# Kernel optimization log

Hardware: AMD Instinct MI355X
Metric: run time of the kernel (lower is better)

The kernel has to match this reference:

```python
import jax, jax.numpy as jnp
import numpy as np

_DN = ('NDHWC', 'DHWIO', 'NDHWC')

def _deconv(x, w, b, stride):
    # kernel-3 transposed conv; SAME padding -> out spatial = in * stride
    y = jax.lax.conv_transpose(x, w, strides=(stride, stride, stride),
                               padding='SAME', dimension_numbers=_DN)
    return y + b


def setup_inputs() -> dict:
    key = jax.random.key(0)
    ks = jax.random.split(key, 14)
    C = 128

    def w(k, cin, cout):
        std = 1.0 / np.sqrt(27.0 * cin)  # fan-in init, kernel 3^3
        return jax.random.normal(k, (3, 3, 3, cin, cout), jnp.float32) * std

    def b(k, cout):
        return jax.random.normal(k, (cout,), jnp.float32) * 0.01

    return {
        'x':   jax.random.normal(ks[0], (1, 8, 8, 8, C), jnp.float32),
        'w0':  w(ks[1], C, C),  'b0':  b(ks[2], C),
        'w00': w(ks[3], C, C),  'b00': b(ks[4], C),
        'w1':  w(ks[5], C, C),  'b1':  b(ks[6], C),
        'w10': w(ks[7], C, C),  'b10': b(ks[8], C),
        'w2':  w(ks[9], C, 64), 'b2':  b(ks[10], 64),
        'w20': w(ks[11], 64, 3), 'b20': b(ks[12], 3),
    }


def reference(x, w0, b0, w00, b00, w1, b1, w10, b10, w2, b2, w20, b20):
    # deconv0 (stride 2) -> deconv0_0 (stride 1) -> ReLU
    out = jax.nn.relu(_deconv(_deconv(x, w0, b0, 2), w00, b00, 1))
    # deconv1 (stride 2) -> deconv1_0 (stride 1) -> ReLU
    out = jax.nn.relu(_deconv(_deconv(out, w1, b1, 2), w10, b10, 1))
    # deconv2 (stride 2, C->64) -> deconv2_0 (stride 1, 64->3)
    out = _deconv(_deconv(out, w2, b2, 2), w20, b20, 1)
    return out
```

## Files before the change

### kernel.cpp

```cpp
#include <hip/hip_runtime.h>


typedef __attribute__((ext_vector_type(8))) short bf16x8;
typedef __attribute__((ext_vector_type(8))) _Float16 f16x8;
typedef __attribute__((ext_vector_type(4))) float f32x4;
typedef unsigned short u16;

__device__ __forceinline__ u16 f2bf(float f) {
    unsigned u = __builtin_bit_cast(unsigned, f);
    u += 0x7fffu + ((u >> 16) & 1u);
    return (u16)(u >> 16);
}
__device__ __forceinline__ float bf2f(u16 h) {
    unsigned u = ((unsigned)h) << 16;
    return __builtin_bit_cast(float, u);
}
__device__ __forceinline__ void split_store(float v, u16* ph, u16* pl) {
    u16 h = f2bf(v);
    *ph = h;
    *pl = f2bf(v - bf2f(h));
}
__device__ __forceinline__ u16 f2h(float v) {
    return __builtin_bit_cast(u16, (_Float16)v);
}
__device__ __forceinline__ int rfl(int v) { return __builtin_amdgcn_readfirstlane(v); }
__device__ __forceinline__ int swz(int bx, int G) { return (bx & 7) * (G >> 3) + (bx >> 3); }

__global__ __launch_bounds__(256) void pack_all(
    const float* __restrict__ x, float* __restrict__ zf,
    u16* __restrict__ Xh, u16* __restrict__ Xl,
    const float* __restrict__ w0_, const float* __restrict__ w1_,
    const float* __restrict__ w2_, const float* __restrict__ w3_,
    const float* __restrict__ w4_, const float* __restrict__ w5_,
    u16* s0h, u16* s0l, u16* s1h, u16* s1l, u16* s2h, u16* s2l,
    u16* s3h, u16* s3l, u16* s4h, u16* s4l, u16* s5h, u16* s5l)
{
    if (blockIdx.y == 6) {
        if (blockIdx.x < 64) {
            const int i = (blockIdx.x * 256 + threadIdx.x) * 4;
            const float4 v = *(const float4*)(x + i);
            split_store(v.x, Xh + i,     Xl + i);
            split_store(v.y, Xh + i + 1, Xl + i + 1);
            split_store(v.z, Xh + i + 2, Xl + i + 2);
            split_store(v.w, Xh + i + 3, Xl + i + 3);
        } else if (blockIdx.x == 64) {
            ((float4*)zf)[threadIdx.x] = make_float4(0.f, 0.f, 0.f, 0.f);
        }
        return;
    }
    const float* w; u16 *bh, *bl; int Cin, Cout, nNt;
    switch (blockIdx.y) {
        case 0: w = w0_; bh = s0h; bl = s0l; Cin = 128; Cout = 128; nNt = 8; break;
        case 1: w = w1_; bh = s1h; bl = s1l; Cin = 128; Cout = 128; nNt = 8; break;
        case 2: w = w2_; bh = s2h; bl = s2l; Cin = 128; Cout = 128; nNt = 8; break;
        case 3: w = w3_; bh = s3h; bl = s3l; Cin = 128; Cout = 128; nNt = 8; break;
        case 4: w = w4_; bh = s4h; bl = s4l; Cin = 128; Cout = 64;  nNt = 4; break;
        default:w = w5_; bh = s5h; bl = s5l; Cin = 64;  Cout = 3;   nNt = 1; break;
    }
    const bool f16 = (blockIdx.y == 5);
    const int KC = Cin >> 5;
    const int total = 27 * nNt * KC * 64;
    int t = blockIdx.x * 256 + threadIdx.x;
    if (t >= total) return;
    const int lane = t & 63;
    int r = t >> 6;
    const int kc = r % KC; r /= KC;
    const int nt = r % nNt; r /= nNt;
    const int tap = r;
    const int n  = nt * 16 + (lane & 15);
    const int k0 = kc * 32 + (lane >> 4) * 8;
    const size_t o = (size_t)t * 8;
    for (int j = 0; j < 8; ++j) {
        float v = (n < Cout) ? w[((size_t)tap * Cin + k0 + j) * Cout + n] : 0.f;
        if (f16) {
            const _Float16 h = (_Float16)v;
            bh[o + j] = __builtin_bit_cast(u16, h);
            bl[o + j] = f2h(v - (float)h);
        } else {
            const u16 h = f2bf(v);
            bh[o + j] = h;
            bl[o + j] = f2bf(v - bf2f(h));
        }
    }
}

template<int CIN, int MT, int NT, bool RELU>
__global__ __launch_bounds__(64) void conv_s1_mfma(
    const u16* __restrict__ Ah, const u16* __restrict__ Al,
    const u16* __restrict__ Bh, const u16* __restrict__ Bl,
    const float* __restrict__ bias, const u16* __restrict__ Z,
    u16* __restrict__ Yh, u16* __restrict__ Yl,
    int D, int lD, int Cout, int nNtTot)
{
    constexpr int KC = CIN >> 5;
    const int lane = threadIdx.x;
    const int ml = lane & 15, kq = lane >> 4;
    const int M0 = swz(blockIdx.x, gridDim.x) * (MT * 16);
    const int N0t = blockIdx.y * NT;

    int vw[MT], vh[MT], vd[MT];
    #pragma unroll
    for (int mt = 0; mt < MT; ++mt) {
        const int vox = M0 + mt * 16 + ml;
        vw[mt] = vox & (D - 1); vh[mt] = (vox >> lD) & (D - 1); vd[mt] = vox >> (2 * lD);
    }

    f32x4 acc[MT][NT];
    #pragma unroll
    for (int nt = 0; nt < NT; ++nt) {
        const float bv = bias[(N0t + nt) * 16 + ml];
        #pragma unroll
        for (int mt = 0; mt < MT; ++mt) acc[mt][nt] = (f32x4){bv, bv, bv, bv};
    }

    const u16 *pah[MT], *pal[MT];
    size_t fb;
    auto set_tap = [&](int tap) {
        const int kd = tap / 9, kh = (tap % 9) / 3, kw = tap % 3;
        #pragma unroll
        for (int mt = 0; mt < MT; ++mt) {
            const int id = vd[mt] + kd - 1, ih = vh[mt] + kh - 1, iw = vw[mt] + kw - 1;
            const bool v = (unsigned)id < (unsigned)D && (unsigned)ih < (unsigned)D &&
                           (unsigned)iw < (unsigned)D;
            const size_t off = (size_t)((id * D + ih) * D + iw) * CIN;
            pah[mt] = v ? Ah + off : Z;
            pal[mt] = v ? Al + off : Z;
        }
        fb = ((size_t)tap * nNtTot + N0t) * KC;
    };

    bf16x8 fah[2][MT], fal[2][MT], fbh[2][NT], fbl[2][NT];
    auto load_frags = [&](int buf, int kc) {
        const int ko = kc * 32 + kq * 8;
        #pragma unroll
        for (int mt = 0; mt < MT; ++mt) {
            fah[buf][mt] = *(const bf16x8*)(pah[mt] + ko);
            fal[buf][mt] = *(const bf16x8*)(pal[mt] + ko);
        }
        #pragma unroll
        for (int nt = 0; nt < NT; ++nt) {
            const size_t fo = (fb + (size_t)nt * KC + kc) * 512 + lane * 8;
            fbh[buf][nt] = *(const bf16x8*)(Bh + fo);
            fbl[buf][nt] = *(const bf16x8*)(Bl + fo);
        }
    };

    set_tap(0);
    load_frags(0, 0);

    for (int tap = 0; tap < 27; ++tap) {
        #pragma unroll
        for (int kc = 0; kc < KC; ++kc) {
            const int cur = kc & 1, nxt = cur ^ 1;
            if (kc + 1 < KC) {
                load_frags(nxt, kc + 1);
            } else {
                set_tap(tap < 26 ? tap + 1 : 26);
                load_frags(nxt, 0);
            }
            #pragma unroll
            for (int mt = 0; mt < MT; ++mt)
            #pragma unroll
            for (int nt = 0; nt < NT; ++nt) {
                acc[mt][nt] = __builtin_amdgcn_mfma_f32_16x16x32_bf16(fah[cur][mt], fbh[cur][nt], acc[mt][nt], 0, 0, 0);
                acc[mt][nt] = __builtin_amdgcn_mfma_f32_16x16x32_bf16(fah[cur][mt], fbl[cur][nt], acc[mt][nt], 0, 0, 0);
                acc[mt][nt] = __builtin_amdgcn_mfma_f32_16x16x32_bf16(fal[cur][mt], fbh[cur][nt], acc[mt][nt], 0, 0, 0);
            }
        }
    }

    #pragma unroll
    for (int mt = 0; mt < MT; ++mt) {
        const int vox0 = M0 + mt * 16 + kq * 4;
        #pragma unroll
        for (int nt = 0; nt < NT; ++nt) {
            const int co = (N0t + nt) * 16 + ml;
            #pragma unroll
            for (int r = 0; r < 4; ++r) {
                float v = acc[mt][nt][r];
                if (RELU) v = fmaxf(v, 0.f);
                const size_t yo = (size_t)(vox0 + r) * Cout + co;
                split_store(v, Yh + yo, Yl + yo);
            }
        }
    }
}

template<int D, int R, bool RELU>
__global__ __launch_bounds__(256) void conv_s1_lds(
    const u16* __restrict__ Ah, const u16* __restrict__ Al,
    const u16* __restrict__ Bh, const u16* __restrict__ Bl,
    const float* __restrict__ bias,
    u16* __restrict__ Yh, u16* __restrict__ Yl)
{
    constexpr int KC  = 4;
    constexpr int SH  = R + 2;
    constexpr int SW  = D + 2;
    constexpr int VST = 72;
    __shared__ u16 sm[3 * SH * SW * VST];

    const int tid  = threadIdx.x;
    const int lane = tid & 63, widx = tid >> 6;
    const int ml = lane & 15, kq = lane >> 4;

    const int bpp = D / R;
    const int lb  = swz(blockIdx.x, gridDim.x);
    const int d   = lb / bpp;
    const int h0  = (lb % bpp) * R;
    const int N0  = widx * 2;

    f32x4 acc[4][2];
    #pragma unroll
    for (int nt = 0; nt < 2; ++nt) {
        const float bv = bias[(N0 + nt) * 16 + ml];
        #pragma unroll
        for (int mt = 0; mt < 4; ++mt) acc[mt][nt] = (f32x4){bv, bv, bv, bv};
    }

    for (int i = tid; i < 3 * SH * 2 * 9; i += 256) {
        const int slot = i / 9, c8 = i % 9;
        const int side = slot & 1, rr = slot >> 1;
        const int dd = rr / SH, hh = rr % SH;
        *(bf16x8*)(sm + ((dd * SH + hh) * SW + (side ? SW - 1 : 0)) * VST + c8 * 8) =
            (bf16x8){0,0,0,0,0,0,0,0};
    }

    bf16x8 cbh[2], cbl[2], nbh[2], nbl[2];
    auto loadB = [&](bf16x8 (&dh)[2], bf16x8 (&dl)[2], int kc, int tap) {
        #pragma unroll
        for (int nt = 0; nt < 2; ++nt) {
            const size_t fo = (((size_t)tap * 8 + N0 + nt) * KC + kc) * 512 + lane * 8;
            dh[nt] = *(const bf16x8*)(Bh + fo);
            dl[nt] = *(const bf16x8*)(Bl + fo);
        }
    };
    loadB(cbh, cbl, 0, 0);

    for (int kc = 0; kc < KC; ++kc) {
        __syncthreads();
        constexpr int NCH = 3 * SH * D * 8;
        for (int i = tid; i < NCH; i += 256) {
            const int vox = i >> 3, c8 = i & 7;
            const int ww = vox % D;
            const int rr = vox / D;
            const int hh = rr % SH, dd = rr / SH;
            const int pd = d + dd - 1, ph = h0 + hh - 1;
            u16* dst = sm + ((dd * SH + hh) * SW + ww + 1) * VST + c8 * 8;
            if ((unsigned)pd < (unsigned)D && (unsigned)ph < (unsigned)D) {
                const u16* srcb = (c8 < 4) ? Ah : Al;
                const size_t g = ((size_t)(pd * D + ph) * D + ww) * 128 + kc * 32 + (c8 & 3) * 8;
                *(bf16x8*)dst = *(const bf16x8*)(srcb + g);
            } else {
                *(bf16x8*)dst = (bf16x8){0,0,0,0,0,0,0,0};
            }
        }
        __syncthreads();

        for (int tap = 0; tap < 27; ++tap) {
            const int lin = kc * 27 + tap + 1;
            if (lin < KC * 27) loadB(nbh, nbl, lin / 27, lin % 27);
            const int kd = tap / 9, kh = (tap % 9) / 3, kw = tap % 3;
            bf16x8 fa_h[4], fa_l[4];
            #pragma unroll
            for (int mt = 0; mt < 4; ++mt) {
                const int m = mt * 16 + ml;
                const int mh = m / D, mw = m % D;
                const u16* p = sm + (((kd * SH) + (mh + kh)) * SW + (mw + kw)) * VST;
                fa_h[mt] = *(const bf16x8*)(p + kq * 8);
                fa_l[mt] = *(const bf16x8*)(p + 32 + kq * 8);
            }
            #pragma unroll
            for (int mt = 0; mt < 4; ++mt)
            #pragma unroll
            for (int nt = 0; nt < 2; ++nt) {
                acc[mt][nt] = __builtin_amdgcn_mfma_f32_16x16x32_bf16(fa_h[mt], cbh[nt], acc[mt][nt], 0, 0, 0);
                acc[mt][nt] = __builtin_amdgcn_mfma_f32_16x16x32_bf16(fa_h[mt], cbl[nt], acc[mt][nt], 0, 0, 0);
                acc[mt][nt] = __builtin_amdgcn_mfma_f32_16x16x32_bf16(fa_l[mt], cbh[nt], acc[mt][nt], 0, 0, 0);
            }
            #pragma unroll
            for (int nt = 0; nt < 2; ++nt) { cbh[nt] = nbh[nt]; cbl[nt] = nbl[nt]; }
        }
    }

    const size_t M0 = (size_t)(d * D + h0) * D;
    #pragma unroll
    for (int mt = 0; mt < 4; ++mt) {
        #pragma unroll
        for (int nt = 0; nt < 2; ++nt) {
            const int co = (N0 + nt) * 16 + ml;
            #pragma unroll
            for (int r = 0; r < 4; ++r) {
                float v = acc[mt][nt][r];
                if (RELU) v = fmaxf(v, 0.f);
                const size_t yo = (M0 + mt * 16 + kq * 4 + r) * 128 + co;
                split_store(v, Yh + yo, Yl + yo);
            }
        }
    }
}

template<int CIN, int MT, int NT, bool F16OUT = false>
__global__ __launch_bounds__(64) void deconv_s2_mfma(
    const u16* __restrict__ Ah, const u16* __restrict__ Al,
    const u16* __restrict__ Bh, const u16* __restrict__ Bl,
    const float* __restrict__ bias, const u16* __restrict__ Z,
    u16* __restrict__ Yh, u16* __restrict__ Yl,
    int Din, int lD, int Cout, int nNtTot)
{
    constexpr int KC = CIN >> 5;
    const int Dout = 2 * Din;
    const int lane = threadIdx.x;
    const int ml = lane & 15, kq = lane >> 4;
    const int M0 = swz(blockIdx.x, gridDim.x) * (MT * 16);
    const int N0t = blockIdx.y * NT;
    const int par = blockIdx.z;
    const int rd = (par >> 2) & 1, rh = (par >> 1) & 1, rw = par & 1;

    int sw[MT], sh[MT], sd[MT];
    #pragma unroll
    for (int mt = 0; mt < MT; ++mt) {
        const int sv = M0 + mt * 16 + ml;
        sw[mt] = sv & (Din - 1); sh[mt] = (sv >> lD) & (Din - 1); sd[mt] = sv >> (2 * lD);
    }

    f32x4 acc[MT][NT];
    #pragma unroll
    for (int nt = 0; nt < NT; ++nt) {
        const float bv = bias[(N0t + nt) * 16 + ml];
        #pragma unroll
        for (int mt = 0; mt < MT; ++mt) acc[mt][nt] = (f32x4){bv, bv, bv, bv};
    }

    const int lw = rw ? 0 : 1, lh = rh ? 0 : 1, ld2 = rd ? 0 : 1;
    const int ntap = 1 << (lw + lh + ld2);

    const u16 *pah[MT], *pal[MT];
    size_t fb;
    auto set_tap = [&](int t) {
        const int tw_ = t & ((1 << lw) - 1);
        const int th_ = (t >> lw) & ((1 << lh) - 1);
        const int td_ = t >> (lw + lh);
        const int kd = rd ? 1 : (td_ ? 0 : 2);
        const int kh = rh ? 1 : (th_ ? 0 : 2);
        const int kw = rw ? 1 : (tw_ ? 0 : 2);
        const int dd = rd ? 0 : -td_, dh = rh ? 0 : -th_, dw = rw ? 0 : -tw_;
        const int tap = (kd * 3 + kh) * 3 + kw;
        #pragma unroll
        for (int mt = 0; mt < MT; ++mt) {
            const int id = sd[mt] + dd, ih = sh[mt] + dh, iw = sw[mt] + dw;
            const bool v = id >= 0 && ih >= 0 && iw >= 0;
            const size_t off = (size_t)((id * Din + ih) * Din + iw) * CIN;
            pah[mt] = v ? Ah + off : Z;
            pal[mt] = v ? Al + off : Z;
        }
        fb = ((size_t)tap * nNtTot + N0t) * KC;
    };

    bf16x8 fah[2][MT], fal[2][MT], fbh[2][NT], fbl[2][NT];
    auto load_frags = [&](int buf, int kc) {
        const int ko = kc * 32 + kq * 8;
        #pragma unroll
        for (int mt = 0; mt < MT; ++mt) {
            fah[buf][mt] = *(const bf16x8*)(pah[mt] + ko);
            fal[buf][mt] = *(const bf16x8*)(pal[mt] + ko);
        }
        #pragma unroll
        for (int nt = 0; nt < NT; ++nt) {
            const size_t fo = (fb + (size_t)nt * KC + kc) * 512 + lane * 8;
            fbh[buf][nt] = *(const bf16x8*)(Bh + fo);
            fbl[buf][nt] = *(const bf16x8*)(Bl + fo);
        }
    };

    set_tap(0);
    load_frags(0, 0);

    for (int t = 0; t < ntap; ++t) {
        #pragma unroll
        for (int kc = 0; kc < KC; ++kc) {
            const int cur = kc & 1, nxt = cur ^ 1;
            if (kc + 1 < KC) {
                load_frags(nxt, kc + 1);
            } else {
                set_tap(t + 1 < ntap ? t + 1 : t);
                load_frags(nxt, 0);
            }
            #pragma unroll
            for (int mt = 0; mt < MT; ++mt)
            #pragma unroll
            for (int nt = 0; nt < NT; ++nt) {
                acc[mt][nt] = __builtin_amdgcn_mfma_f32_16x16x32_bf16(fah[cur][mt], fbh[cur][nt], acc[mt][nt], 0, 0, 0);
                acc[mt][nt] = __builtin_amdgcn_mfma_f32_16x16x32_bf16(fah[cur][mt], fbl[cur][nt], acc[mt][nt], 0, 0, 0);
                acc[mt][nt] = __builtin_amdgcn_mfma_f32_16x16x32_bf16(fal[cur][mt], fbh[cur][nt], acc[mt][nt], 0, 0, 0);
            }
        }
    }

    #pragma unroll
    for (int mt = 0; mt < MT; ++mt) {
        #pragma unroll
        for (int r = 0; r < 4; ++r) {
            const int sv = M0 + mt * 16 + kq * 4 + r;
            const int svw = sv & (Din - 1), svh = (sv >> lD) & (Din - 1), svd = sv >> (2 * lD);
            const int od = 2 * svd + rd, oh = 2 * svh + rh, ow = 2 * svw + rw;
            const size_t yb = (size_t)((od * Dout + oh) * Dout + ow) * Cout;
            #pragma unroll
            for (int nt = 0; nt < NT; ++nt) {
                const int co = (N0t + nt) * 16 + ml;
                if (F16OUT) Yh[yb + co] = f2h(acc[mt][nt][r]);
                else        split_store(acc[mt][nt][r], Yh + yb + co, Yl + yb + co);
            }
        }
    }
}

#define L5_VST 40
#define L5_RST (66 * L5_VST)
__global__ __launch_bounds__(256) void conv_c3_lds(
    const u16* __restrict__ A,
    const u16* __restrict__ Bh, const u16* __restrict__ Bl,
    const float* __restrict__ bias, float* __restrict__ out)
{
    __shared__ u16 sm[6 * L5_RST];

    const int tid  = threadIdx.x;
    const int lane = tid & 63, widx = tid >> 6;
    const int ml = lane & 15, kq = lane >> 4;

    const int lb = swz(blockIdx.x, gridDim.x);
    const int d  = lb >> 4;
    const int h0 = (lb & 15) * 4;

    const float bv = (ml < 3) ? bias[ml] : 0.f;
    f32x4 acc[4];
    #pragma unroll
    for (int mt = 0; mt < 4; ++mt) acc[mt] = (f32x4){bv, bv, bv, bv};

    f16x8 cbh, cbl, nbh, nbl;
    auto loadB = [&](f16x8& dh, f16x8& dl, int tap, int kc) {
        const size_t fo = ((size_t)tap * 2 + kc) * 512 + lane * 8;
        dh = *(const f16x8*)(Bh + fo);
        dl = *(const f16x8*)(Bl + fo);
    };
    loadB(cbh, cbl, 0, 0);

    for (int kd = 0; kd < 3; ++kd) {
        const int pd = d + kd - 1;
        const bool vpd = (unsigned)pd < 64u;
        for (int kc = 0; kc < 2; ++kc) {
            __syncthreads();
            #pragma unroll
            for (int i = 0; i < 6; ++i) {
                const int c = tid + 256 * i;
                const int r = c >> 8;
                const int rem = c & 255;
                const int vox = rem >> 2, c8 = rem & 3;
                const int hh = h0 - 1 + r;
                u16* dst = sm + r * L5_RST + (vox + 1) * L5_VST + c8 * 8;
                if (vpd && (unsigned)hh < 64u) {
                    const size_t g = (size_t)((pd * 64 + hh) * 64 + vox) * 64
                                   + kc * 32 + c8 * 8;
                    *(f16x8*)dst = *(const f16x8*)(A + g);
                } else {
                    *(f16x8*)dst = (f16x8){0,0,0,0,0,0,0,0};
                }
            }
            if (tid < 48) {
                const int r = tid >> 3, side = (tid >> 2) & 1, c8 = tid & 3;
                *(f16x8*)(sm + r * L5_RST + (side ? 65 : 0) * L5_VST + c8 * 8) =
                    (f16x8){0,0,0,0,0,0,0,0};
            }
            __syncthreads();

            #pragma unroll
            for (int t = 0; t < 9; ++t) {
                {
                    int lin = (kd * 2 + kc) * 9 + t + 1;
                    if (lin > 53) lin = 53;
                    const int Pn = lin / 9, tn = lin - Pn * 9;
                    loadB(nbh, nbl, (Pn >> 1) * 9 + tn, Pn & 1);
                }
                const int kh = t / 3, kw = t - kh * 3;
                const int slot = widx + kh;
                #pragma unroll
                for (int mt = 0; mt < 4; ++mt) {
                    const u16* p = sm + slot * L5_RST + (mt * 16 + ml + kw) * L5_VST;
                    const f16x8 af = *(const f16x8*)(p + kq * 8);
                    acc[mt] = __builtin_amdgcn_mfma_f32_16x16x32_f16(af, cbh, acc[mt], 0, 0, 0);
                    acc[mt] = __builtin_amdgcn_mfma_f32_16x16x32_f16(af, cbl, acc[mt], 0, 0, 0);
                }
                cbh = nbh; cbl = nbl;
            }
        }
    }

    if (ml < 3) {
        const int h = h0 + widx;
        const size_t vb = (size_t)(d * 64 + h) * 64;
        #pragma unroll
        for (int mt = 0; mt < 4; ++mt)
        #pragma unroll
        for (int r = 0; r < 4; ++r)
            out[(vb + mt * 16 + kq * 4 + r) * 3 + ml] = acc[mt][r];
    }
}

extern "C" void kernel_launch(void* const* d_in, const int* in_sizes, int n_in,
                              void* d_out, int out_size, void* d_ws, size_t ws_size,
                              hipStream_t stream)
{
    const float* x   = (const float*)d_in[0];
    const float* w0  = (const float*)d_in[1];  const float* b0  = (const float*)d_in[2];
    const float* w00 = (const float*)d_in[3];  const float* b00 = (const float*)d_in[4];
    const float* w1  = (const float*)d_in[5];  const float* b1  = (const float*)d_in[6];
    const float* w10 = (const float*)d_in[7];  const float* b10 = (const float*)d_in[8];
    const float* w2  = (const float*)d_in[9];  const float* b2  = (const float*)d_in[10];
    const float* w20 = (const float*)d_in[11]; const float* b20 = (const float*)d_in[12];
    float* out = (float*)d_out;

    char* ws = (char*)d_ws;
    float* zf = (float*)ws;
    u16*   Z  = (u16*)ws;
    u16* S4h = (u16*)(ws + 4096);
    u16* S4l = S4h + 221184;
    u16* S5h = S4l + 221184;
    u16* S5l = S5h + 27648;
    u16* Qh  = (u16*)(ws + 1048576);
    u16* Ql  = Qh + 4194304;
    u16* Ph  = (u16*)(ws + 17825792);
    u16* Pl  = Ph + 16777216;
    u16* S1h = (u16*)(ws + 60817408);
    u16* S1l = S1h + 442368;
    u16* S2h = S1l + 442368;
    u16* S2l = S2h + 442368;
    u16* S3h = S2l + 442368;
    u16* S3l = S3h + 442368;
    u16* S0h = S3l + 442368;
    u16* S0l = S0h + 442368;
    u16* Xh  = S0l + 442368;
    u16* Xl  = Xh + 65536;

    pack_all<<<dim3(216, 7), 256, 0, stream>>>(x, zf, Xh, Xl,
        w0, w00, w1, w10, w2, w20,
        S0h, S0l, S1h, S1l, S2h, S2l, S3h, S3l, S4h, S4l, S5h, S5l);

    deconv_s2_mfma<128, 2, 4><<<dim3(16, 2, 8), 64, 0, stream>>>(
        Xh, Xl, S0h, S0l, b0, Z, Ph, Pl, 8, 3, 128, 8);

    conv_s1_mfma<128, 1, 2, true><<<dim3(256, 4), 64, 0, stream>>>(
        Ph, Pl, S1h, S1l, b00, Z, Qh, Ql, 16, 4, 128, 8);

    deconv_s2_mfma<128, 2, 4><<<dim3(128, 2, 8), 64, 0, stream>>>(
        Qh, Ql, S2h, S2l, b1, Z, Ph, Pl, 16, 4, 128, 8);

    conv_s1_lds<32, 2, true><<<dim3(512), 256, 0, stream>>>(
        Ph, Pl, S3h, S3l, b10, Qh, Ql);

    deconv_s2_mfma<128, 4, 4, true><<<dim3(512, 1, 8), 64, 0, stream>>>(
        Qh, Ql, S4h, S4l, b2, Z, Ph, Pl, 32, 5, 64, 4);

    conv_c3_lds<<<dim3(1024), 256, 0, stream>>>(Ph, S5h, S5l, b20, out);
}
```

Before: 369.9 us.

## Switch intermediate activations to single fp16 with split fp16 weights

Intermediate activations between layers are now stored as one fp16 array instead of a bf16 hi/lo pair. Weights for layers 1-5 are packed as fp16 hi/lo. Each K step now issues two f16 MFMAs instead of three bf16 MFMAs, and activation loads, stores and LDS staging are halved. The cost is lower activation precision (fp16 mantissa and range instead of about 16-bit split bf16), which could affect accuracy.

```diff
diff --git a/kernel.cpp b/kernel.cpp
--- a/kernel.cpp
+++ b/kernel.cpp
@@ -23,7 +23,6 @@
 __device__ __forceinline__ u16 f2h(float v) {
     return __builtin_bit_cast(u16, (_Float16)v);
 }
-__device__ __forceinline__ int rfl(int v) { return __builtin_amdgcn_readfirstlane(v); }
 __device__ __forceinline__ int swz(int bx, int G) { return (bx & 7) * (G >> 3) + (bx >> 3); }
 
 __global__ __launch_bounds__(256) void pack_all(
@@ -57,7 +56,7 @@
         case 4: w = w4_; bh = s4h; bl = s4l; Cin = 128; Cout = 64;  nNt = 4; break;
         default:w = w5_; bh = s5h; bl = s5l; Cin = 64;  Cout = 3;   nNt = 1; break;
     }
-    const bool f16 = (blockIdx.y == 5);
+    const bool f16 = (blockIdx.y >= 1);
     const int KC = Cin >> 5;
     const int total = 27 * nNt * KC * 64;
     int t = blockIdx.x * 256 + threadIdx.x;
@@ -84,228 +83,12 @@
     }
 }
 
-template<int CIN, int MT, int NT, bool RELU>
-__global__ __launch_bounds__(64) void conv_s1_mfma(
+template<int CIN, int MT, int NT>
+__global__ __launch_bounds__(64) void deconv_s2_bf16(
     const u16* __restrict__ Ah, const u16* __restrict__ Al,
     const u16* __restrict__ Bh, const u16* __restrict__ Bl,
     const float* __restrict__ bias, const u16* __restrict__ Z,
-    u16* __restrict__ Yh, u16* __restrict__ Yl,
-    int D, int lD, int Cout, int nNtTot)
-{
-    constexpr int KC = CIN >> 5;
-    const int lane = threadIdx.x;
-    const int ml = lane & 15, kq = lane >> 4;
-    const int M0 = swz(blockIdx.x, gridDim.x) * (MT * 16);
-    const int N0t = blockIdx.y * NT;
-
-    int vw[MT], vh[MT], vd[MT];
-    #pragma unroll
-    for (int mt = 0; mt < MT; ++mt) {
-        const int vox = M0 + mt * 16 + ml;
-        vw[mt] = vox & (D - 1); vh[mt] = (vox >> lD) & (D - 1); vd[mt] = vox >> (2 * lD);
-    }
-
-    f32x4 acc[MT][NT];
-    #pragma unroll
-    for (int nt = 0; nt < NT; ++nt) {
-        const float bv = bias[(N0t + nt) * 16 + ml];
-        #pragma unroll
-        for (int mt = 0; mt < MT; ++mt) acc[mt][nt] = (f32x4){bv, bv, bv, bv};
-    }
-
-    const u16 *pah[MT], *pal[MT];
-    size_t fb;
-    auto set_tap = [&](int tap) {
-        const int kd = tap / 9, kh = (tap % 9) / 3, kw = tap % 3;
-        #pragma unroll
-        for (int mt = 0; mt < MT; ++mt) {
-            const int id = vd[mt] + kd - 1, ih = vh[mt] + kh - 1, iw = vw[mt] + kw - 1;
-            const bool v = (unsigned)id < (unsigned)D && (unsigned)ih < (unsigned)D &&
-                           (unsigned)iw < (unsigned)D;
-            const size_t off = (size_t)((id * D + ih) * D + iw) * CIN;
-            pah[mt] = v ? Ah + off : Z;
-            pal[mt] = v ? Al + off : Z;
-        }
-        fb = ((size_t)tap * nNtTot + N0t) * KC;
-    };
-
-    bf16x8 fah[2][MT], fal[2][MT], fbh[2][NT], fbl[2][NT];
-    auto load_frags = [&](int buf, int kc) {
-        const int ko = kc * 32 + kq * 8;
-        #pragma unroll
-        for (int mt = 0; mt < MT; ++mt) {
-            fah[buf][mt] = *(const bf16x8*)(pah[mt] + ko);
-            fal[buf][mt] = *(const bf16x8*)(pal[mt] + ko);
-        }
-        #pragma unroll
-        for (int nt = 0; nt < NT; ++nt) {
-            const size_t fo = (fb + (size_t)nt * KC + kc) * 512 + lane * 8;
-            fbh[buf][nt] = *(const bf16x8*)(Bh + fo);
-            fbl[buf][nt] = *(const bf16x8*)(Bl + fo);
-        }
-    };
-
-    set_tap(0);
-    load_frags(0, 0);
-
-    for (int tap = 0; tap < 27; ++tap) {
-        #pragma unroll
-        for (int kc = 0; kc < KC; ++kc) {
-            const int cur = kc & 1, nxt = cur ^ 1;
-            if (kc + 1 < KC) {
-                load_frags(nxt, kc + 1);
-            } else {
-                set_tap(tap < 26 ? tap + 1 : 26);
-                load_frags(nxt, 0);
-            }
-            #pragma unroll
-            for (int mt = 0; mt < MT; ++mt)
-            #pragma unroll
-            for (int nt = 0; nt < NT; ++nt) {
-                acc[mt][nt] = __builtin_amdgcn_mfma_f32_16x16x32_bf16(fah[cur][mt], fbh[cur][nt], acc[mt][nt], 0, 0, 0);
-                acc[mt][nt] = __builtin_amdgcn_mfma_f32_16x16x32_bf16(fah[cur][mt], fbl[cur][nt], acc[mt][nt], 0, 0, 0);
-                acc[mt][nt] = __builtin_amdgcn_mfma_f32_16x16x32_bf16(fal[cur][mt], fbh[cur][nt], acc[mt][nt], 0, 0, 0);
-            }
-        }
-    }
-
-    #pragma unroll
-    for (int mt = 0; mt < MT; ++mt) {
-        const int vox0 = M0 + mt * 16 + kq * 4;
-        #pragma unroll
-        for (int nt = 0; nt < NT; ++nt) {
-            const int co = (N0t + nt) * 16 + ml;
-            #pragma unroll
-            for (int r = 0; r < 4; ++r) {
-                float v = acc[mt][nt][r];
-                if (RELU) v = fmaxf(v, 0.f);
-                const size_t yo = (size_t)(vox0 + r) * Cout + co;
-                split_store(v, Yh + yo, Yl + yo);
-            }
-        }
-    }
-}
-
-template<int D, int R, bool RELU>
-__global__ __launch_bounds__(256) void conv_s1_lds(
-    const u16* __restrict__ Ah, const u16* __restrict__ Al,
-    const u16* __restrict__ Bh, const u16* __restrict__ Bl,
-    const float* __restrict__ bias,
-    u16* __restrict__ Yh, u16* __restrict__ Yl)
-{
-    constexpr int KC  = 4;
-    constexpr int SH  = R + 2;
-    constexpr int SW  = D + 2;
-    constexpr int VST = 72;
-    __shared__ u16 sm[3 * SH * SW * VST];
-
-    const int tid  = threadIdx.x;
-    const int lane = tid & 63, widx = tid >> 6;
-    const int ml = lane & 15, kq = lane >> 4;
-
-    const int bpp = D / R;
-    const int lb  = swz(blockIdx.x, gridDim.x);
-    const int d   = lb / bpp;
-    const int h0  = (lb % bpp) * R;
-    const int N0  = widx * 2;
-
-    f32x4 acc[4][2];
-    #pragma unroll
-    for (int nt = 0; nt < 2; ++nt) {
-        const float bv = bias[(N0 + nt) * 16 + ml];
-        #pragma unroll
-        for (int mt = 0; mt < 4; ++mt) acc[mt][nt] = (f32x4){bv, bv, bv, bv};
-    }
-
-    for (int i = tid; i < 3 * SH * 2 * 9; i += 256) {
-        const int slot = i / 9, c8 = i % 9;
-        const int side = slot & 1, rr = slot >> 1;
-        const int dd = rr / SH, hh = rr % SH;
-        *(bf16x8*)(sm + ((dd * SH + hh) * SW + (side ? SW - 1 : 0)) * VST + c8 * 8) =
-            (bf16x8){0,0,0,0,0,0,0,0};
-    }
-
-    bf16x8 cbh[2], cbl[2], nbh[2], nbl[2];
-    auto loadB = [&](bf16x8 (&dh)[2], bf16x8 (&dl)[2], int kc, int tap) {
-        #pragma unroll
-        for (int nt = 0; nt < 2; ++nt) {
-            const size_t fo = (((size_t)tap * 8 + N0 + nt) * KC + kc) * 512 + lane * 8;
-            dh[nt] = *(const bf16x8*)(Bh + fo);
-            dl[nt] = *(const bf16x8*)(Bl + fo);
-        }
-    };
-    loadB(cbh, cbl, 0, 0);
-
-    for (int kc = 0; kc < KC; ++kc) {
-        __syncthreads();
-        constexpr int NCH = 3 * SH * D * 8;
-        for (int i = tid; i < NCH; i += 256) {
-            const int vox = i >> 3, c8 = i & 7;
-            const int ww = vox % D;
-            const int rr = vox / D;
-            const int hh = rr % SH, dd = rr / SH;
-            const int pd = d + dd - 1, ph = h0 + hh - 1;
-            u16* dst = sm + ((dd * SH + hh) * SW + ww + 1) * VST + c8 * 8;
-            if ((unsigned)pd < (unsigned)D && (unsigned)ph < (unsigned)D) {
-                const u16* srcb = (c8 < 4) ? Ah : Al;
-                const size_t g = ((size_t)(pd * D + ph) * D + ww) * 128 + kc * 32 + (c8 & 3) * 8;
-                *(bf16x8*)dst = *(const bf16x8*)(srcb + g);
-            } else {
-                *(bf16x8*)dst = (bf16x8){0,0,0,0,0,0,0,0};
-            }
-        }
-        __syncthreads();
-
-        for (int tap = 0; tap < 27; ++tap) {
-            const int lin = kc * 27 + tap + 1;
-            if (lin < KC * 27) loadB(nbh, nbl, lin / 27, lin % 27);
-            const int kd = tap / 9, kh = (tap % 9) / 3, kw = tap % 3;
-            bf16x8 fa_h[4], fa_l[4];
-            #pragma unroll
-            for (int mt = 0; mt < 4; ++mt) {
-                const int m = mt * 16 + ml;
-                const int mh = m / D, mw = m % D;
-                const u16* p = sm + (((kd * SH) + (mh + kh)) * SW + (mw + kw)) * VST;
-                fa_h[mt] = *(const bf16x8*)(p + kq * 8);
-                fa_l[mt] = *(const bf16x8*)(p + 32 + kq * 8);
-            }
-            #pragma unroll
-            for (int mt = 0; mt < 4; ++mt)
-            #pragma unroll
-            for (int nt = 0; nt < 2; ++nt) {
-                acc[mt][nt] = __builtin_amdgcn_mfma_f32_16x16x32_bf16(fa_h[mt], cbh[nt], acc[mt][nt], 0, 0, 0);
-                acc[mt][nt] = __builtin_amdgcn_mfma_f32_16x16x32_bf16(fa_h[mt], cbl[nt], acc[mt][nt], 0, 0, 0);
-                acc[mt][nt] = __builtin_amdgcn_mfma_f32_16x16x32_bf16(fa_l[mt], cbh[nt], acc[mt][nt], 0, 0, 0);
-            }
-            #pragma unroll
-            for (int nt = 0; nt < 2; ++nt) { cbh[nt] = nbh[nt]; cbl[nt] = nbl[nt]; }
-        }
-    }
-
-    const size_t M0 = (size_t)(d * D + h0) * D;
-    #pragma unroll
-    for (int mt = 0; mt < 4; ++mt) {
-        #pragma unroll
-        for (int nt = 0; nt < 2; ++nt) {
-            const int co = (N0 + nt) * 16 + ml;
-            #pragma unroll
-            for (int r = 0; r < 4; ++r) {
-                float v = acc[mt][nt][r];
-                if (RELU) v = fmaxf(v, 0.f);
-                const size_t yo = (M0 + mt * 16 + kq * 4 + r) * 128 + co;
-                split_store(v, Yh + yo, Yl + yo);
-            }
-        }
-    }
-}
-
-template<int CIN, int MT, int NT, bool F16OUT = false>
-__global__ __launch_bounds__(64) void deconv_s2_mfma(
-    const u16* __restrict__ Ah, const u16* __restrict__ Al,
-    const u16* __restrict__ Bh, const u16* __restrict__ Bl,
-    const float* __restrict__ bias, const u16* __restrict__ Z,
-    u16* __restrict__ Yh, u16* __restrict__ Yl,
-    int Din, int lD, int Cout, int nNtTot)
+    u16* __restrict__ Y, int Din, int lD, int Cout, int nNtTot)
 {
     constexpr int KC = CIN >> 5;
     const int Dout = 2 * Din;
@@ -405,10 +188,313 @@
             const int od = 2 * svd + rd, oh = 2 * svh + rh, ow = 2 * svw + rw;
             const size_t yb = (size_t)((od * Dout + oh) * Dout + ow) * Cout;
             #pragma unroll
+            for (int nt = 0; nt < NT; ++nt)
+                Y[yb + (N0t + nt) * 16 + ml] = f2h(acc[mt][nt][r]);
+        }
+    }
+}
+
+template<int CIN, int MT, int NT, bool RELU>
+__global__ __launch_bounds__(64) void conv_s1_f16(
+    const u16* __restrict__ A, const u16* __restrict__ Bh, const u16* __restrict__ Bl,
+    const float* __restrict__ bias, const u16* __restrict__ Z,
+    u16* __restrict__ Y, int D, int lD, int Cout, int nNtTot)
+{
+    constexpr int KC = CIN >> 5;
+    const int lane = threadIdx.x;
+    const int ml = lane & 15, kq = lane >> 4;
+    const int M0 = swz(blockIdx.x, gridDim.x) * (MT * 16);
+    const int N0t = blockIdx.y * NT;
+
+    int vw[MT], vh[MT], vd[MT];
+    #pragma unroll
+    for (int mt = 0; mt < MT; ++mt) {
+        const int vox = M0 + mt * 16 + ml;
+        vw[mt] = vox & (D - 1); vh[mt] = (vox >> lD) & (D - 1); vd[mt] = vox >> (2 * lD);
+    }
+
+    f32x4 acc[MT][NT];
+    #pragma unroll
+    for (int nt = 0; nt < NT; ++nt) {
+        const float bv = bias[(N0t + nt) * 16 + ml];
+        #pragma unroll
+        for (int mt = 0; mt < MT; ++mt) acc[mt][nt] = (f32x4){bv, bv, bv, bv};
+    }
+
+    const u16* pa[MT];
+    size_t fb;
+    auto set_tap = [&](int tap) {
+        const int kd = tap / 9, kh = (tap % 9) / 3, kw = tap % 3;
+        #pragma unroll
+        for (int mt = 0; mt < MT; ++mt) {
+            const int id = vd[mt] + kd - 1, ih = vh[mt] + kh - 1, iw = vw[mt] + kw - 1;
+            const bool v = (unsigned)id < (unsigned)D && (unsigned)ih < (unsigned)D &&
+                           (unsigned)iw < (unsigned)D;
+            pa[mt] = v ? A + (size_t)((id * D + ih) * D + iw) * CIN : Z;
+        }
+        fb = ((size_t)tap * nNtTot + N0t) * KC;
+    };
+
+    f16x8 fa[2][MT], fbh[2][NT], fbl[2][NT];
+    auto load_frags = [&](int buf, int kc) {
+        const int ko = kc * 32 + kq * 8;
+        #pragma unroll
+        for (int mt = 0; mt < MT; ++mt)
+            fa[buf][mt] = *(const f16x8*)(pa[mt] + ko);
+        #pragma unroll
+        for (int nt = 0; nt < NT; ++nt) {
+            const size_t fo = (fb + (size_t)nt * KC + kc) * 512 + lane * 8;
+            fbh[buf][nt] = *(const f16x8*)(Bh + fo);
+            fbl[buf][nt] = *(const f16x8*)(Bl + fo);
+        }
+    };
+
+    set_tap(0);
+    load_frags(0, 0);
+
+    for (int tap = 0; tap < 27; ++tap) {
+        #pragma unroll
+        for (int kc = 0; kc < KC; ++kc) {
+            const int cur = kc & 1, nxt = cur ^ 1;
+            if (kc + 1 < KC) {
+                load_frags(nxt, kc + 1);
+            } else {
+                set_tap(tap < 26 ? tap + 1 : 26);
+                load_frags(nxt, 0);
+            }
+            #pragma unroll
+            for (int mt = 0; mt < MT; ++mt)
+            #pragma unroll
             for (int nt = 0; nt < NT; ++nt) {
-                const int co = (N0t + nt) * 16 + ml;
-                if (F16OUT) Yh[yb + co] = f2h(acc[mt][nt][r]);
-                else        split_store(acc[mt][nt][r], Yh + yb + co, Yl + yb + co);
+                acc[mt][nt] = __builtin_amdgcn_mfma_f32_16x16x32_f16(fa[cur][mt], fbh[cur][nt], acc[mt][nt], 0, 0, 0);
+                acc[mt][nt] = __builtin_amdgcn_mfma_f32_16x16x32_f16(fa[cur][mt], fbl[cur][nt], acc[mt][nt], 0, 0, 0);
+            }
+        }
+    }
+
+    #pragma unroll
+    for (int mt = 0; mt < MT; ++mt) {
+        const int vox0 = M0 + mt * 16 + kq * 4;
+        #pragma unroll
+        for (int nt = 0; nt < NT; ++nt) {
+            const int co = (N0t + nt) * 16 + ml;
+            #pragma unroll
+            for (int r = 0; r < 4; ++r) {
+                float v = acc[mt][nt][r];
+                if (RELU) v = fmaxf(v, 0.f);
+                Y[(size_t)(vox0 + r) * Cout + co] = f2h(v);
+            }
+        }
+    }
+}
+
+template<int CIN, int MT, int NT>
+__global__ __launch_bounds__(64) void deconv_s2_f16(
+    const u16* __restrict__ A, const u16* __restrict__ Bh, const u16* __restrict__ Bl,
+    const float* __restrict__ bias, const u16* __restrict__ Z,
+    u16* __restrict__ Y, int Din, int lD, int Cout, int nNtTot)
+{
+    constexpr int KC = CIN >> 5;
+    const int Dout = 2 * Din;
+    const int lane = threadIdx.x;
+    const int ml = lane & 15, kq = lane >> 4;
+    const int M0 = swz(blockIdx.x, gridDim.x) * (MT * 16);
+    const int N0t = blockIdx.y * NT;
+    const int par = blockIdx.z;
+    const int rd = (par >> 2) & 1, rh = (par >> 1) & 1, rw = par & 1;
+
+    int sw[MT], sh[MT], sd[MT];
+    #pragma unroll
+    for (int mt = 0; mt < MT; ++mt) {
+        const int sv = M0 + mt * 16 + ml;
+        sw[mt] = sv & (Din - 1); sh[mt] = (sv >> lD) & (Din - 1); sd[mt] = sv >> (2 * lD);
+    }
+
+    f32x4 acc[MT][NT];
+    #pragma unroll
+    for (int nt = 0; nt < NT; ++nt) {
+        const float bv = bias[(N0t + nt) * 16 + ml];
+        #pragma unroll
+        for (int mt = 0; mt < MT; ++mt) acc[mt][nt] = (f32x4){bv, bv, bv, bv};
+    }
+
+    const int lw = rw ? 0 : 1, lh = rh ? 0 : 1, ld2 = rd ? 0 : 1;
+    const int ntap = 1 << (lw + lh + ld2);
+
+    const u16* pa[MT];
+    size_t fb;
+    auto set_tap = [&](int t) {
+        const int tw_ = t & ((1 << lw) - 1);
+        const int th_ = (t >> lw) & ((1 << lh) - 1);
+        const int td_ = t >> (lw + lh);
+        const int kd = rd ? 1 : (td_ ? 0 : 2);
+        const int kh = rh ? 1 : (th_ ? 0 : 2);
+        const int kw = rw ? 1 : (tw_ ? 0 : 2);
+        const int dd = rd ? 0 : -td_, dh = rh ? 0 : -th_, dw = rw ? 0 : -tw_;
+        const int tap = (kd * 3 + kh) * 3 + kw;
+        #pragma unroll
+        for (int mt = 0; mt < MT; ++mt) {
+            const int id = sd[mt] + dd, ih = sh[mt] + dh, iw = sw[mt] + dw;
+            const bool v = id >= 0 && ih >= 0 && iw >= 0;
+            pa[mt] = v ? A + (size_t)((id * Din + ih) * Din + iw) * CIN : Z;
+        }
+        fb = ((size_t)tap * nNtTot + N0t) * KC;
+    };
+
+    f16x8 fa[2][MT], fbh[2][NT], fbl[2][NT];
+    auto load_frags = [&](int buf, int kc) {
+        const int ko = kc * 32 + kq * 8;
+        #pragma unroll
+        for (int mt = 0; mt < MT; ++mt)
+            fa[buf][mt] = *(const f16x8*)(pa[mt] + ko);
+        #pragma unroll
+        for (int nt = 0; nt < NT; ++nt) {
+            const size_t fo = (fb + (size_t)nt * KC + kc) * 512 + lane * 8;
+            fbh[buf][nt] = *(const f16x8*)(Bh + fo);
+            fbl[buf][nt] = *(const f16x8*)(Bl + fo);
+        }
+    };
+
+    set_tap(0);
+    load_frags(0, 0);
+
+    for (int t = 0; t < ntap; ++t) {
+        #pragma unroll
+        for (int kc = 0; kc < KC; ++kc) {
+            const int cur = kc & 1, nxt = cur ^ 1;
+            if (kc + 1 < KC) {
+                load_frags(nxt, kc + 1);
+            } else {
+                set_tap(t + 1 < ntap ? t + 1 : t);
+                load_frags(nxt, 0);
+            }
+            #pragma unroll
+            for (int mt = 0; mt < MT; ++mt)
+            #pragma unroll
+            for (int nt = 0; nt < NT; ++nt) {
+                acc[mt][nt] = __builtin_amdgcn_mfma_f32_16x16x32_f16(fa[cur][mt], fbh[cur][nt], acc[mt][nt], 0, 0, 0);
+                acc[mt][nt] = __builtin_amdgcn_mfma_f32_16x16x32_f16(fa[cur][mt], fbl[cur][nt], acc[mt][nt], 0, 0, 0);
+            }
+        }
+    }
+
+    #pragma unroll
+    for (int mt = 0; mt < MT; ++mt) {
+        #pragma unroll
+        for (int r = 0; r < 4; ++r) {
+            const int sv = M0 + mt * 16 + kq * 4 + r;
+            const int svw = sv & (Din - 1), svh = (sv >> lD) & (Din - 1), svd = sv >> (2 * lD);
+            const int od = 2 * svd + rd, oh = 2 * svh + rh, ow = 2 * svw + rw;
+            const size_t yb = (size_t)((od * Dout + oh) * Dout + ow) * Cout;
+            #pragma unroll
+            for (int nt = 0; nt < NT; ++nt)
+                Y[yb + (N0t + nt) * 16 + ml] = f2h(acc[mt][nt][r]);
+        }
+    }
+}
+
+template<int D, int R, bool RELU>
+__global__ __launch_bounds__(256) void conv_s1_lds_f16(
+    const u16* __restrict__ A, const u16* __restrict__ Bh, const u16* __restrict__ Bl,
+    const float* __restrict__ bias, u16* __restrict__ Y)
+{
+    constexpr int KC  = 4;
+    constexpr int SH  = R + 2;
+    constexpr int SW  = D + 2;
+    constexpr int VST = 40;
+    __shared__ u16 sm[3 * SH * SW * VST];
+
+    const int tid  = threadIdx.x;
+    const int lane = tid & 63, widx = tid >> 6;
+    const int ml = lane & 15, kq = lane >> 4;
+
+    const int bpp = D / R;
+    const int lb  = swz(blockIdx.x, gridDim.x);
+    const int d   = lb / bpp;
+    const int h0  = (lb % bpp) * R;
+    const int N0  = widx * 2;
+
+    f32x4 acc[4][2];
+    #pragma unroll
+    for (int nt = 0; nt < 2; ++nt) {
+        const float bv = bias[(N0 + nt) * 16 + ml];
+        #pragma unroll
+        for (int mt = 0; mt < 4; ++mt) acc[mt][nt] = (f32x4){bv, bv, bv, bv};
+    }
+
+    for (int i = tid; i < 3 * SH * 2 * 4; i += 256) {
+        const int slot = i >> 2, c8 = i & 3;
+        const int side = slot & 1, rr = slot >> 1;
+        const int dd = rr / SH, hh = rr % SH;
+        *(f16x8*)(sm + ((dd * SH + hh) * SW + (side ? SW - 1 : 0)) * VST + c8 * 8) =
+            (f16x8){0,0,0,0,0,0,0,0};
+    }
+
+    f16x8 cbh[2], cbl[2], nbh[2], nbl[2];
+    auto loadB = [&](f16x8 (&dh)[2], f16x8 (&dl)[2], int kc, int tap) {
+        #pragma unroll
+        for (int nt = 0; nt < 2; ++nt) {
+            const size_t fo = (((size_t)tap * 8 + N0 + nt) * KC + kc) * 512 + lane * 8;
+            dh[nt] = *(const f16x8*)(Bh + fo);
+            dl[nt] = *(const f16x8*)(Bl + fo);
+        }
+    };
+    loadB(cbh, cbl, 0, 0);
+
+    for (int kc = 0; kc < KC; ++kc) {
+        __syncthreads();
+        constexpr int NCH = 3 * SH * D * 4;
+        for (int i = tid; i < NCH; i += 256) {
+            const int vox = i >> 2, c8 = i & 3;
+            const int ww = vox % D;
+            const int rr = vox / D;
+            const int hh = rr % SH, dd = rr / SH;
+            const int pd = d + dd - 1, ph = h0 + hh - 1;
+            u16* dst = sm + ((dd * SH + hh) * SW + ww + 1) * VST + c8 * 8;
+            if ((unsigned)pd < (unsigned)D && (unsigned)ph < (unsigned)D) {
+                const size_t g = ((size_t)(pd * D + ph) * D + ww) * 128 + kc * 32 + c8 * 8;
+                *(f16x8*)dst = *(const f16x8*)(A + g);
+            } else {
+                *(f16x8*)dst = (f16x8){0,0,0,0,0,0,0,0};
+            }
+        }
+        __syncthreads();
+
+        for (int tap = 0; tap < 27; ++tap) {
+            const int lin = kc * 27 + tap + 1;
+            if (lin < KC * 27) loadB(nbh, nbl, lin / 27, lin % 27);
+            const int kd = tap / 9, kh = (tap % 9) / 3, kw = tap % 3;
+            f16x8 fa[4];
+            #pragma unroll
+            for (int mt = 0; mt < 4; ++mt) {
+                const int m = mt * 16 + ml;
+                const int mh = m / D, mw = m % D;
+                fa[mt] = *(const f16x8*)(sm + (((kd * SH) + (mh + kh)) * SW + (mw + kw)) * VST
+                                          + kq * 8);
+            }
+            #pragma unroll
+            for (int mt = 0; mt < 4; ++mt)
+            #pragma unroll
+            for (int nt = 0; nt < 2; ++nt) {
+                acc[mt][nt] = __builtin_amdgcn_mfma_f32_16x16x32_f16(fa[mt], cbh[nt], acc[mt][nt], 0, 0, 0);
+                acc[mt][nt] = __builtin_amdgcn_mfma_f32_16x16x32_f16(fa[mt], cbl[nt], acc[mt][nt], 0, 0, 0);
+            }
+            #pragma unroll
+            for (int nt = 0; nt < 2; ++nt) { cbh[nt] = nbh[nt]; cbl[nt] = nbl[nt]; }
+        }
+    }
+
+    const size_t M0 = (size_t)(d * D + h0) * D;
+    #pragma unroll
+    for (int mt = 0; mt < 4; ++mt) {
+        #pragma unroll
+        for (int nt = 0; nt < 2; ++nt) {
+            const int co = (N0 + nt) * 16 + ml;
+            #pragma unroll
+            for (int r = 0; r < 4; ++r) {
+                float v = acc[mt][nt][r];
+                if (RELU) v = fmaxf(v, 0.f);
+                Y[(M0 + mt * 16 + kq * 4 + r) * 128 + co] = f2h(v);
             }
         }
     }
@@ -544,20 +630,20 @@
         w0, w00, w1, w10, w2, w20,
         S0h, S0l, S1h, S1l, S2h, S2l, S3h, S3l, S4h, S4l, S5h, S5l);
 
-    deconv_s2_mfma<128, 2, 4><<<dim3(16, 2, 8), 64, 0, stream>>>(
-        Xh, Xl, S0h, S0l, b0, Z, Ph, Pl, 8, 3, 128, 8);
-
-    conv_s1_mfma<128, 1, 2, true><<<dim3(256, 4), 64, 0, stream>>>(
-        Ph, Pl, S1h, S1l, b00, Z, Qh, Ql, 16, 4, 128, 8);
-
-    deconv_s2_mfma<128, 2, 4><<<dim3(128, 2, 8), 64, 0, stream>>>(
-        Qh, Ql, S2h, S2l, b1, Z, Ph, Pl, 16, 4, 128, 8);
-
-    conv_s1_lds<32, 2, true><<<dim3(512), 256, 0, stream>>>(
-        Ph, Pl, S3h, S3l, b10, Qh, Ql);
-
-    deconv_s2_mfma<128, 4, 4, true><<<dim3(512, 1, 8), 64, 0, stream>>>(
-        Qh, Ql, S4h, S4l, b2, Z, Ph, Pl, 32, 5, 64, 4);
+    deconv_s2_bf16<128, 2, 4><<<dim3(16, 2, 8), 64, 0, stream>>>(
+        Xh, Xl, S0h, S0l, b0, Z, Ph, 8, 3, 128, 8);
+
+    conv_s1_f16<128, 1, 2, true><<<dim3(256, 4), 64, 0, stream>>>(
+        Ph, S1h, S1l, b00, Z, Qh, 16, 4, 128, 8);
+
+    deconv_s2_f16<128, 2, 4><<<dim3(128, 2, 8), 64, 0, stream>>>(
+        Qh, S2h, S2l, b1, Z, Ph, 16, 4, 128, 8);
+
+    conv_s1_lds_f16<32, 2, true><<<dim3(512), 256, 0, stream>>>(
+        Ph, S3h, S3l, b10, Qh);
+
+    deconv_s2_f16<128, 4, 4><<<dim3(512, 1, 8), 64, 0, stream>>>(
+        Qh, S4h, S4l, b2, Z, Ph, 32, 5, 64, 4);
 
     conv_c3_lds<<<dim3(1024), 256, 0, stream>>>(Ph, S5h, S5l, b20, out);
 }
```

Result: faster. 309.6 us (-16.3%).
